# Kernel tuning notes

Measured on AMD Instinct MI355X. Metric: run time of the kernel, lower is better.

## Reference

```python
import jax, jax.numpy as jnp
import numpy as np

B, C, P, H, W = 8, 256, 64, 64, 64


def conv2d(x, w, b, pad):
    y = jax.lax.conv_general_dilated(
        x, w, window_strides=(1, 1), padding=[(pad, pad), (pad, pad)],
        dimension_numbers=("NCHW", "OIHW", "NCHW"))
    return y + b[None, :, None, None]


def setup_inputs() -> dict:
    key = jax.random.key(0)
    ks = jax.random.split(key, 9)
    x = jax.random.normal(ks[0], (B, C, H, W), dtype=jnp.float32)
    # conv weights, OIHW layout; scale ~ kaiming-ish
    w_top = jax.random.normal(ks[1], (P, C, 1, 1), jnp.float32) * (1.0 / np.sqrt(C))
    b_top = jnp.zeros((P,), jnp.float32)
    w_center = jax.random.normal(ks[2], (P, C, 1, 1), jnp.float32) * (1.0 / np.sqrt(C))
    b_center = jnp.zeros((P,), jnp.float32)
    w_bottom = jax.random.normal(ks[3], (C, C, 3, 3), jnp.float32) * (1.0 / np.sqrt(9 * C))
    b_bottom = jnp.zeros((C,), jnp.float32)
    w_out = jax.random.normal(ks[4], (C, C, 3, 3), jnp.float32) * (1.0 / np.sqrt(9 * C))
    b_out = jnp.zeros((C,), jnp.float32)
    return {"x": x, "w_top": w_top, "b_top": b_top, "w_center": w_center,
            "b_center": b_center, "w_bottom": w_bottom, "b_bottom": b_bottom,
            "w_out": w_out, "b_out": b_out}


def reference(x, w_top, b_top, w_center, b_center, w_bottom, b_bottom, w_out, b_out):
    b, c, h, w = x.shape
    hw = h * w
    x_top = conv2d(x, w_top, b_top, 0).reshape(b, -1, hw)          # [B, P, HW]
    x_center = conv2d(x, w_center, b_center, 0).reshape(b, -1, hw)  # [B, P, HW]
    x_center = jnp.swapaxes(x_center, 1, 2)                          # [B, HW, P]
    x_bottom = conv2d(x, w_bottom, b_bottom, 1).reshape(b, c, hw)
    x_bottom = jnp.swapaxes(x_bottom, 1, 2)                          # [B, HW, C]
    sp_map = jnp.einsum("bnp,bpm->bnm", x_center, x_top)            # [B, HW, HW]
    # NOTE: softmax is GLOBAL over the flattened HW*HW map per batch element,
    # not per-row (faithful to original Softmax(dim=1) on view(bsize, -1)).
    sp_map = jax.nn.softmax(sp_map.reshape(b, -1), axis=1).reshape(b, hw, hw)
    sp_map = jnp.einsum("bnm,bmc->bnc", sp_map, x_bottom)           # [B, HW, C]
    # NOTE: original does .reshape(b, C, h, w) on a [B, HW, C] tensor (no
    # transpose) -- replicate that exact memory reinterpretation.
    sp_map = sp_map.reshape(b, c, h, w)
    return conv2d(x + sp_map, w_out, b_out, 1)
```

## Files before the change

kernel.cpp:

```cpp
#include <hip/hip_runtime.h>
#include <hip/hip_bf16.h>
#include <type_traits>

constexpr int B_ = 8, C_ = 256, P_ = 64, H_ = 64, W_ = 64, HW_ = 4096;

typedef __attribute__((ext_vector_type(8))) short short8;
typedef __attribute__((ext_vector_type(4))) short short4v;
typedef __attribute__((ext_vector_type(4))) float f32x4;

__device__ __forceinline__ short bfbits(float f) {
    __hip_bfloat16 h = __float2bfloat16(f);
    return *reinterpret_cast<short*>(&h);
}
__device__ __forceinline__ float bf2f(short s) {
    __hip_bfloat16 h = *reinterpret_cast<__hip_bfloat16*>(&s);
    return (float)h;
}

#define GLL16(gsrc, ldst)                                                      \
    __builtin_amdgcn_global_load_lds(                                         \
        (const __attribute__((address_space(1))) void*)(gsrc),                \
        (__attribute__((address_space(3))) void*)(ldst), 16, 0, 0)


__global__ __launch_bounds__(256) void k_prep_w(
    const float* __restrict__ w, short8* __restrict__ wbP)
{
    const int idx = blockIdx.x * 256 + threadIdx.x;
    const int lane = idx & 63, cot = (idx >> 6) & 15;
    const int cb = (idx >> 10) & 7, tap = idx >> 13;
    const int lm = lane & 15, lq = lane >> 4;
    const int co = cot * 16 + lm, ci0 = cb * 32 + lq * 8;
    short8 v;
#pragma unroll
    for (int k = 0; k < 8; ++k)
        v[k] = bfbits(w[(co * 256 + ci0 + k) * 9 + tap]);
    wbP[idx] = v;
}

__global__ __launch_bounds__(256) void k_cvt_bf16(
    const float* __restrict__ x, short8* __restrict__ xB)
{
    const size_t i = ((size_t)blockIdx.x * 256 + threadIdx.x) * 16;
    short8 o[2];
#pragma unroll
    for (int q = 0; q < 2; ++q) {
#pragma unroll
        for (int j = 0; j < 2; ++j) {
            const float4 v = *reinterpret_cast<const float4*>(&x[i + q * 8 + j * 4]);
            o[q][j * 4 + 0] = bfbits(v.x);
            o[q][j * 4 + 1] = bfbits(v.y);
            o[q][j * 4 + 2] = bfbits(v.z);
            o[q][j * 4 + 3] = bfbits(v.w);
        }
    }
    short8* dp = (short8*)&xB[i >> 3];
    dp[0] = o[0];
    dp[1] = o[1];
}

__global__ __launch_bounds__(256) void k_pack_xb(
    const __hip_bfloat16* __restrict__ xb, short8* __restrict__ xbP)
{
    const int tid = blockIdx.x * 256 + threadIdx.x;
    const int lane = tid & 63, wid = tid >> 6;
    const int ct = wid & 15, g = (wid >> 4) & 127, b = wid >> 11;
    const int c = ct * 16 + (lane >> 2);
    const int mo = g * 32 + (lane & 3) * 8;
    const short8 v = *reinterpret_cast<const short8*>(
        &xb[((size_t)(b * 256 + c)) * HW_ + mo]);
    xbP[(size_t)wid * 64 + (lane & 3) * 16 + (lane >> 2)] = v;
}

__global__ __launch_bounds__(256) void k_conv1x1(
    const float* __restrict__ x,
    const float* __restrict__ w_top, const float* __restrict__ b_top,
    const float* __restrict__ w_cen, const float* __restrict__ b_cen,
    short8* __restrict__ xtPh, short8* __restrict__ xtPl,
    short8* __restrict__ xcPh, short8* __restrict__ xcPl)
{
    const int b = blockIdx.z;
    const int n = blockIdx.x * 256 + threadIdx.x;
    const int conv = blockIdx.y >> 2, pq = blockIdx.y & 3;
    const int p0 = pq * 16;
    const float* w    = conv ? w_cen : w_top;
    const float* bias = conv ? b_cen : b_top;
    short8* oh = conv ? xcPh : xtPh;
    short8* ol = conv ? xcPl : xtPl;

    const float* xp = x + (size_t)b * C_ * HW_ + n;
    float acc[16];
#pragma unroll
    for (int p = 0; p < 16; ++p) acc[p] = 0.f;

    for (int c = 0; c < C_; c += 4) {
        const float xv0 = xp[(size_t)(c + 0) * HW_];
        const float xv1 = xp[(size_t)(c + 1) * HW_];
        const float xv2 = xp[(size_t)(c + 2) * HW_];
        const float xv3 = xp[(size_t)(c + 3) * HW_];
#pragma unroll
        for (int p = 0; p < 16; ++p) {
            const float4 wv = *reinterpret_cast<const float4*>(&w[(p0 + p) * C_ + c]);
            float a = acc[p];
            a = fmaf(wv.x, xv0, a);
            a = fmaf(wv.y, xv1, a);
            a = fmaf(wv.z, xv2, a);
            a = fmaf(wv.w, xv3, a);
            acc[p] = a;
        }
    }
    const int nt = n >> 4, lmn = n & 15;
    const size_t obase = ((size_t)(b * 256 + nt) * 2 + (pq >> 1)) * 64 + lmn;
#pragma unroll
    for (int jj = 0; jj < 2; ++jj) {
        short8 vh, vl;
#pragma unroll
        for (int k = 0; k < 8; ++k) {
            const float v = acc[jj * 8 + k] + bias[p0 + jj * 8 + k];
            const short hb = bfbits(v);
            vh[k] = hb;
            vl[k] = bfbits(v - bf2f(hb));
        }
        const size_t idx = obase + (size_t)(((pq & 1) * 2 + jj) * 16);
        oh[idx] = vh;
        ol[idx] = vl;
    }
}

template <typename OT>
__global__ __launch_bounds__(512, 4) void k_conv3x3_mfma(
    const short* __restrict__ xin, const short8* __restrict__ wbP,
    const float* __restrict__ bias, OT* __restrict__ out)
{
    __shared__ __align__(16) short Xs[3][66][40];
    const int lin = blockIdx.x;
    const int b = lin & 7, h = lin >> 3;
    const int t = threadIdx.x;
    const int wave = t >> 6, lane = t & 63;
    const int lm = lane & 15, lq = lane >> 4;
    const int cobase = wave * 32;
    const int cot0 = wave * 2;

    f32x4 acc[4][2];
#pragma unroll
    for (int i = 0; i < 4; ++i)
#pragma unroll
        for (int j = 0; j < 2; ++j) acc[i][j] = f32x4{0.f, 0.f, 0.f, 0.f};

    if (t < 192) {
        const int r = t >> 6, cc = t & 31, side = (t >> 5) & 1;
        Xs[r][side ? 65 : 0][cc] = 0;
    }

    const short* xbase = xin + (size_t)b * C_ * HW_;

    for (int cb = 0; cb < 8; ++cb) {
        const int ci0 = cb * 32;
        __syncthreads();
#pragma unroll
        for (int it = 0; it < 3; ++it) {
            const int idx = it * 512 + t;
            const int r = idx >> 9, ci = (idx >> 4) & 31, wq = idx & 15;
            const int hh = h + r - 1;
            short4v v = {0, 0, 0, 0};
            if (hh >= 0 && hh < H_)
                v = *reinterpret_cast<const short4v*>(
                    &xbase[(size_t)(ci0 + ci) * HW_ + hh * W_ + wq * 4]);
            Xs[r][1 + wq * 4 + 0][ci] = v[0];
            Xs[r][1 + wq * 4 + 1][ci] = v[1];
            Xs[r][1 + wq * 4 + 2][ci] = v[2];
            Xs[r][1 + wq * 4 + 3][ci] = v[3];
        }
        __syncthreads();

#pragma unroll 3
        for (int tap = 0; tap < 9; ++tap) {
            const int dh = tap / 3;
            const int dw = tap % 3;
            const short8* wp = wbP + ((size_t)(tap * 8 + cb)) * 1024 + lane;
            short8 af[2];
            af[0] = wp[(cot0 + 0) * 64];
            af[1] = wp[(cot0 + 1) * 64];
            short8 bf[4];
#pragma unroll
            for (int nt = 0; nt < 4; ++nt)
                bf[nt] = *reinterpret_cast<const short8*>(
                    &Xs[dh][nt * 16 + lm + dw][lq * 8]);
#pragma unroll
            for (int nt = 0; nt < 4; ++nt)
#pragma unroll
                for (int ct = 0; ct < 2; ++ct)
                    acc[nt][ct] = __builtin_amdgcn_mfma_f32_16x16x32_bf16(
                        af[ct], bf[nt], acc[nt][ct], 0, 0, 0);
        }
    }

#pragma unroll
    for (int nt = 0; nt < 4; ++nt) {
        const int pos = h * W_ + nt * 16 + lm;
#pragma unroll
        for (int ct = 0; ct < 2; ++ct) {
            const int co = cobase + ct * 16 + lq * 4;
#pragma unroll
            for (int r = 0; r < 4; ++r) {
                const float v = acc[nt][ct][r] + bias[co + r];
                if constexpr (std::is_same<OT, __hip_bfloat16>::value)
                    out[((size_t)(b * C_ + co + r)) * HW_ + pos] = __float2bfloat16(v);
                else
                    out[((size_t)(b * C_ + co + r)) * HW_ + pos] = v;
            }
        }
    }
}

__global__ __launch_bounds__(512, 2) void k_attn_mfma(
    const short8* __restrict__ xtPh, const short8* __restrict__ xtPl,
    const short8* __restrict__ xcPh, const short8* __restrict__ xcPl,
    const short8* __restrict__ xbP, float* __restrict__ O,
    float* __restrict__ Z)
{
    extern __shared__ __align__(16) char smem[];
    short8* XTs = (short8*)smem;
    short8* XBs = (short8*)(smem + 32768);
    short8* Ps8 = (short8*)(smem + 98304);
    short4v* Ps4 = (short4v*)(smem + 98304);
    float* zred = (float*)(smem + 114688);

    const int lin = blockIdx.x;
    const int b = lin & 7, nblk = lin >> 3;
    const int n0 = nblk * 128;

    const int t = threadIdx.x, wv = t >> 6, lane = t & 63;
    const int lm = lane & 15, lq = lane >> 4;
    const int mh = wv >> 2, nq2 = wv & 3;
    const int nq = wv >> 2, cq = wv & 3;

    short8 cB2[2][2][2];
#pragma unroll
    for (int ntile = 0; ntile < 2; ++ntile) {
        const int gt = nblk * 8 + nq2 * 2 + ntile;
        const size_t base = ((size_t)(b * 256 + gt) * 2) * 64 + lane;
        cB2[ntile][0][0] = xcPh[base];
        cB2[ntile][1][0] = xcPh[base + 64];
        cB2[ntile][0][1] = xcPl[base];
        cB2[ntile][1][1] = xcPl[base + 64];
    }
    asm volatile("s_waitcnt vmcnt(0)" ::: "memory");

    auto stage = [&](int smt, int bufi) {
        short8* XT = XTs + bufi * 1024;
        short8* XB = XBs + bufi * 2048;
        const size_t abase = ((size_t)(b * 512 + smt * 8)) * 64;
#pragma unroll
        for (int k = 0; k < 2; ++k) {
            const int c = wv * 2 + k, ms = c >> 2, part = c & 3;
            const short8* src = (part < 2 ? xtPh : xtPl)
                                + abase + ms * 128 + (part & 1) * 64 + lane;
            GLL16(src, XT + c * 64);
        }
        const size_t p8 = ((size_t)(b * 2048 + smt * 32)) * 64;
#pragma unroll
        for (int k = 0; k < 4; ++k) {
            const int e = k * 512 + wv * 64;
            GLL16(xbP + p8 + e + lane, XB + e);
        }
    };
    stage(0, 0);

    f32x4 acc[4][4];
#pragma unroll
    for (int i = 0; i < 4; ++i)
#pragma unroll
        for (int jj = 0; jj < 4; ++jj) acc[i][jj] = f32x4{0.f, 0.f, 0.f, 0.f};
    float zp = 0.f;

    for (int mt = 0; mt < 64; ++mt) {
        const int cur = mt & 1;
        asm volatile("s_waitcnt vmcnt(4)" ::: "memory");
        __builtin_amdgcn_sched_barrier(0);
        __builtin_amdgcn_s_barrier();
        __builtin_amdgcn_sched_barrier(0);
        stage((mt + 1) & 63, cur ^ 1);

        const short8* XT = XTs + cur * 1024;
#pragma unroll
        for (int ms2 = 0; ms2 < 2; ++ms2) {
            const int ms = mh * 2 + ms2;
            const short8 aH0 = XT[(ms * 4 + 0) * 64 + lane];
            const short8 aH1 = XT[(ms * 4 + 1) * 64 + lane];
            const short8 aL0 = XT[(ms * 4 + 2) * 64 + lane];
            const short8 aL1 = XT[(ms * 4 + 3) * 64 + lane];
#pragma unroll
            for (int ntile = 0; ntile < 2; ++ntile) {
                f32x4 s = {0.f, 0.f, 0.f, 0.f};
                __builtin_amdgcn_s_setprio(1);
                s = __builtin_amdgcn_mfma_f32_16x16x32_bf16(aH0, cB2[ntile][0][0], s, 0, 0, 0);
                s = __builtin_amdgcn_mfma_f32_16x16x32_bf16(aH1, cB2[ntile][1][0], s, 0, 0, 0);
                s = __builtin_amdgcn_mfma_f32_16x16x32_bf16(aH0, cB2[ntile][0][1], s, 0, 0, 0);
                s = __builtin_amdgcn_mfma_f32_16x16x32_bf16(aH1, cB2[ntile][1][1], s, 0, 0, 0);
                s = __builtin_amdgcn_mfma_f32_16x16x32_bf16(aL0, cB2[ntile][0][0], s, 0, 0, 0);
                s = __builtin_amdgcn_mfma_f32_16x16x32_bf16(aL1, cB2[ntile][1][0], s, 0, 0, 0);
                __builtin_amdgcn_s_setprio(0);
                const float e0 = __expf(s[0]), e1 = __expf(s[1]);
                const float e2 = __expf(s[2]), e3 = __expf(s[3]);
                zp += (e0 + e1) + (e2 + e3);
                short4v pk = { bfbits(e0), bfbits(e1), bfbits(e2), bfbits(e3) };
                const int T = nq2 * 2 + ntile;
                const int lqp = (ms & 1) * 2 + (lq >> 1);
                Ps4[(((T * 2 + mh) * 64) + lqp * 16 + lm) * 2 + (lq & 1)] = pk;
            }
        }
        asm volatile("s_waitcnt vmcnt(6) lgkmcnt(0)" ::: "memory");
        __builtin_amdgcn_sched_barrier(0);
        __builtin_amdgcn_s_barrier();
        __builtin_amdgcn_sched_barrier(0);

        const short8* XB = XBs + cur * 2048;
        short8 vb0[4], vb1[4];
#pragma unroll
        for (int q4 = 0; q4 < 4; ++q4) {
            const int ct = cq * 4 + q4;
            vb0[q4] = XB[ct * 64 + lane];
            vb1[q4] = XB[1024 + ct * 64 + lane];
        }
#pragma unroll
        for (int nt2 = 0; nt2 < 4; ++nt2) {
            const int T = nq * 4 + nt2;
            const short8 pa0 = Ps8[(T * 2 + 0) * 64 + lane];
            const short8 pa1 = Ps8[(T * 2 + 1) * 64 + lane];
            __builtin_amdgcn_s_setprio(1);
#pragma unroll
            for (int q4 = 0; q4 < 4; ++q4) {
                acc[nt2][q4] = __builtin_amdgcn_mfma_f32_16x16x32_bf16(
                    pa0, vb0[q4], acc[nt2][q4], 0, 0, 0);
                acc[nt2][q4] = __builtin_amdgcn_mfma_f32_16x16x32_bf16(
                    pa1, vb1[q4], acc[nt2][q4], 0, 0, 0);
            }
            __builtin_amdgcn_s_setprio(0);
        }
    }

#pragma unroll
    for (int o = 32; o > 0; o >>= 1) zp += __shfl_down(zp, o, 64);
    if (lane == 0) zred[wv] = zp;
    __syncthreads();
    if (t == 0) {
        float zs = 0.f;
#pragma unroll
        for (int wvi = 0; wvi < 8; ++wvi) zs += zred[wvi];
        atomicAdd(&Z[b], zs);
    }

#pragma unroll
    for (int nt2 = 0; nt2 < 4; ++nt2) {
#pragma unroll
        for (int q4 = 0; q4 < 4; ++q4) {
            const int c = cq * 64 + q4 * 16 + lm;
#pragma unroll
            for (int r = 0; r < 4; ++r) {
                const int n = n0 + (nq * 4 + nt2) * 16 + lq * 4 + r;
                O[((size_t)b * HW_ + n) * C_ + c] = acc[nt2][q4][r];
            }
        }
    }
}

__global__ __launch_bounds__(256) void k_add_bf16(
    const float* __restrict__ x, const float* __restrict__ o,
    const float* __restrict__ Z, short4v* __restrict__ yB)
{
    const int bidx = blockIdx.x;
    const float invZ = 1.0f / Z[bidx >> 10];
    const size_t i = ((size_t)bidx * 256 + threadIdx.x) * 4;
    const float4 a = *reinterpret_cast<const float4*>(&x[i]);
    const float4 b = *reinterpret_cast<const float4*>(&o[i]);
    short4v r{bfbits(fmaf(b.x, invZ, a.x)), bfbits(fmaf(b.y, invZ, a.y)),
              bfbits(fmaf(b.z, invZ, a.z)), bfbits(fmaf(b.w, invZ, a.w))};
    yB[i >> 2] = r;
}

extern "C" void kernel_launch(void* const* d_in, const int* in_sizes, int n_in,
                              void* d_out, int out_size, void* d_ws, size_t ws_size,
                              hipStream_t stream)
{
    const float* x   = (const float*)d_in[0];
    const float* wt  = (const float*)d_in[1];
    const float* bt  = (const float*)d_in[2];
    const float* wc  = (const float*)d_in[3];
    const float* bc  = (const float*)d_in[4];
    const float* wbo = (const float*)d_in[5];
    const float* bbo = (const float*)d_in[6];
    const float* wo  = (const float*)d_in[7];
    const float* bo  = (const float*)d_in[8];
    float* out = (float*)d_out;

    uint8_t* w8 = (uint8_t*)d_ws;
    const size_t MB = 1u << 20;
    short8* xtPh = (short8*)(w8);
    short8* xtPl = (short8*)(w8 + 4 * MB);
    short8* xcPh = (short8*)(w8 + 8 * MB);
    short8* xcPl = (short8*)(w8 + 12 * MB);
    __hip_bfloat16* xbB = (__hip_bfloat16*)(w8 + 16 * MB);
    short8* xbP  = (short8*)(w8 + 32 * MB);
    float*  O    = (float*)(w8 + 48 * MB);
    short8* Wb1  = (short8*)(w8 + 48 * MB);
    short8* xB   = (short8*)(w8 + 64 * MB);
    short8* Wb2  = (short8*)(w8 + 32 * MB);
    short4v* yB  = (short4v*)(w8 + 16 * MB);
    float*  Z    = (float*)(w8 + 80 * MB);

    hipMemsetAsync(Z, 0, B_ * sizeof(float), stream);
    k_prep_w<<<dim3(288), 256, 0, stream>>>(wbo, Wb1);
    k_cvt_bf16<<<dim3(2048), 256, 0, stream>>>(x, xB);
    k_conv1x1<<<dim3(16, 8, 8), 256, 0, stream>>>(x, wt, bt, wc, bc,
                                                  xtPh, xtPl, xcPh, xcPl);
    k_conv3x3_mfma<__hip_bfloat16><<<dim3(512), 512, 0, stream>>>(
        (const short*)xB, Wb1, bbo, xbB);
    k_pack_xb<<<dim3(4096), 256, 0, stream>>>(xbB, xbP);
    k_attn_mfma<<<dim3(256), dim3(512), 114720, stream>>>(xtPh, xtPl, xcPh, xcPl,
                                                          xbP, O, Z);
    k_prep_w<<<dim3(288), 256, 0, stream>>>(wo, Wb2);
    k_add_bf16<<<dim3(8192), 256, 0, stream>>>(x, O, Z, yB);
    k_conv3x3_mfma<float><<<dim3(512), 512, 0, stream>>>(
        (const short*)yB, Wb2, bo, out);
}
```

Measured before the change: 390.0 us.

## Double-buffer conv3x3 LDS input tiles and fuse both 1x1 convs per thread

The 3x3 MFMA conv now keeps two LDS input buffers. It prefetches the next channel block into registers while MFMAs run on the current block, and syncs once per block instead of twice. This aims to hide global load latency behind compute, at the cost of doubled LDS and more registers. Separately, the 1x1 conv kernel computes the top and center projections in one thread so each x value is loaded once, which halves the grid and doubles the accumulators.

```diff
diff --git a/kernel.cpp b/kernel.cpp
--- a/kernel.cpp
+++ b/kernel.cpp
@@ -81,17 +81,13 @@
 {
     const int b = blockIdx.z;
     const int n = blockIdx.x * 256 + threadIdx.x;
-    const int conv = blockIdx.y >> 2, pq = blockIdx.y & 3;
+    const int pq = blockIdx.y;
     const int p0 = pq * 16;
-    const float* w    = conv ? w_cen : w_top;
-    const float* bias = conv ? b_cen : b_top;
-    short8* oh = conv ? xcPh : xtPh;
-    short8* ol = conv ? xcPl : xtPl;
 
     const float* xp = x + (size_t)b * C_ * HW_ + n;
-    float acc[16];
-#pragma unroll
-    for (int p = 0; p < 16; ++p) acc[p] = 0.f;
+    float acc0[16], acc1[16];
+#pragma unroll
+    for (int p = 0; p < 16; ++p) { acc0[p] = 0.f; acc1[p] = 0.f; }
 
     for (int c = 0; c < C_; c += 4) {
         const float xv0 = xp[(size_t)(c + 0) * HW_];
@@ -100,30 +96,37 @@
         const float xv3 = xp[(size_t)(c + 3) * HW_];
 #pragma unroll
         for (int p = 0; p < 16; ++p) {
-            const float4 wv = *reinterpret_cast<const float4*>(&w[(p0 + p) * C_ + c]);
-            float a = acc[p];
-            a = fmaf(wv.x, xv0, a);
-            a = fmaf(wv.y, xv1, a);
-            a = fmaf(wv.z, xv2, a);
-            a = fmaf(wv.w, xv3, a);
-            acc[p] = a;
+            const float4 wv0 = *reinterpret_cast<const float4*>(&w_top[(p0 + p) * C_ + c]);
+            const float4 wv1 = *reinterpret_cast<const float4*>(&w_cen[(p0 + p) * C_ + c]);
+            float a0 = acc0[p], a1 = acc1[p];
+            a0 = fmaf(wv0.x, xv0, a0);  a1 = fmaf(wv1.x, xv0, a1);
+            a0 = fmaf(wv0.y, xv1, a0);  a1 = fmaf(wv1.y, xv1, a1);
+            a0 = fmaf(wv0.z, xv2, a0);  a1 = fmaf(wv1.z, xv2, a1);
+            a0 = fmaf(wv0.w, xv3, a0);  a1 = fmaf(wv1.w, xv3, a1);
+            acc0[p] = a0;  acc1[p] = a1;
         }
     }
     const int nt = n >> 4, lmn = n & 15;
     const size_t obase = ((size_t)(b * 256 + nt) * 2 + (pq >> 1)) * 64 + lmn;
 #pragma unroll
     for (int jj = 0; jj < 2; ++jj) {
-        short8 vh, vl;
+        short8 vh0, vl0, vh1, vl1;
 #pragma unroll
         for (int k = 0; k < 8; ++k) {
-            const float v = acc[jj * 8 + k] + bias[p0 + jj * 8 + k];
-            const short hb = bfbits(v);
-            vh[k] = hb;
-            vl[k] = bfbits(v - bf2f(hb));
+            const float v0 = acc0[jj * 8 + k] + b_top[p0 + jj * 8 + k];
+            const short hb0 = bfbits(v0);
+            vh0[k] = hb0;
+            vl0[k] = bfbits(v0 - bf2f(hb0));
+            const float v1 = acc1[jj * 8 + k] + b_cen[p0 + jj * 8 + k];
+            const short hb1 = bfbits(v1);
+            vh1[k] = hb1;
+            vl1[k] = bfbits(v1 - bf2f(hb1));
         }
         const size_t idx = obase + (size_t)(((pq & 1) * 2 + jj) * 16);
-        oh[idx] = vh;
-        ol[idx] = vl;
+        xtPh[idx] = vh0;
+        xtPl[idx] = vl0;
+        xcPh[idx] = vh1;
+        xcPl[idx] = vl1;
     }
 }
 
@@ -132,7 +135,7 @@
     const short* __restrict__ xin, const short8* __restrict__ wbP,
     const float* __restrict__ bias, OT* __restrict__ out)
 {
-    __shared__ __align__(16) short Xs[3][66][40];
+    __shared__ __align__(16) short Xs[2][3][66][40];
     const int lin = blockIdx.x;
     const int b = lin & 7, h = lin >> 3;
     const int t = threadIdx.x;
@@ -147,16 +150,17 @@
 #pragma unroll
         for (int j = 0; j < 2; ++j) acc[i][j] = f32x4{0.f, 0.f, 0.f, 0.f};
 
-    if (t < 192) {
-        const int r = t >> 6, cc = t & 31, side = (t >> 5) & 1;
-        Xs[r][side ? 65 : 0][cc] = 0;
+    if (t < 384) {
+        const int bufi = t / 192, rem = t % 192;
+        const int r = rem >> 6, cc = rem & 31, side = (rem >> 5) & 1;
+        Xs[bufi][r][side ? 65 : 0][cc] = 0;
     }
 
     const short* xbase = xin + (size_t)b * C_ * HW_;
 
-    for (int cb = 0; cb < 8; ++cb) {
+    short4v pv[3];
+    auto gload = [&](int cb) {
         const int ci0 = cb * 32;
-        __syncthreads();
 #pragma unroll
         for (int it = 0; it < 3; ++it) {
             const int idx = it * 512 + t;
@@ -166,12 +170,28 @@
             if (hh >= 0 && hh < H_)
                 v = *reinterpret_cast<const short4v*>(
                     &xbase[(size_t)(ci0 + ci) * HW_ + hh * W_ + wq * 4]);
-            Xs[r][1 + wq * 4 + 0][ci] = v[0];
-            Xs[r][1 + wq * 4 + 1][ci] = v[1];
-            Xs[r][1 + wq * 4 + 2][ci] = v[2];
-            Xs[r][1 + wq * 4 + 3][ci] = v[3];
-        }
-        __syncthreads();
+            pv[it] = v;
+        }
+    };
+    auto lwrite = [&](int bufi) {
+#pragma unroll
+        for (int it = 0; it < 3; ++it) {
+            const int idx = it * 512 + t;
+            const int r = idx >> 9, ci = (idx >> 4) & 31, wq = idx & 15;
+            Xs[bufi][r][1 + wq * 4 + 0][ci] = pv[it][0];
+            Xs[bufi][r][1 + wq * 4 + 1][ci] = pv[it][1];
+            Xs[bufi][r][1 + wq * 4 + 2][ci] = pv[it][2];
+            Xs[bufi][r][1 + wq * 4 + 3][ci] = pv[it][3];
+        }
+    };
+
+    gload(0);
+    lwrite(0);
+    __syncthreads();
+
+    for (int cb = 0; cb < 8; ++cb) {
+        const int cur = cb & 1;
+        if (cb < 7) gload(cb + 1);
 
 #pragma unroll 3
         for (int tap = 0; tap < 9; ++tap) {
@@ -185,7 +205,7 @@
 #pragma unroll
             for (int nt = 0; nt < 4; ++nt)
                 bf[nt] = *reinterpret_cast<const short8*>(
-                    &Xs[dh][nt * 16 + lm + dw][lq * 8]);
+                    &Xs[cur][dh][nt * 16 + lm + dw][lq * 8]);
 #pragma unroll
             for (int nt = 0; nt < 4; ++nt)
 #pragma unroll
@@ -193,6 +213,9 @@
                     acc[nt][ct] = __builtin_amdgcn_mfma_f32_16x16x32_bf16(
                         af[ct], bf[nt], acc[nt][ct], 0, 0, 0);
         }
+
+        if (cb < 7) lwrite(cur ^ 1);
+        __syncthreads();
     }
 
 #pragma unroll
@@ -412,7 +435,7 @@
     hipMemsetAsync(Z, 0, B_ * sizeof(float), stream);
     k_prep_w<<<dim3(288), 256, 0, stream>>>(wbo, Wb1);
     k_cvt_bf16<<<dim3(2048), 256, 0, stream>>>(x, xB);
-    k_conv1x1<<<dim3(16, 8, 8), 256, 0, stream>>>(x, wt, bt, wc, bc,
+    k_conv1x1<<<dim3(16, 4, 8), 256, 0, stream>>>(x, wt, bt, wc, bc,
                                                   xtPh, xtPl, xcPh, xcPl);
     k_conv3x3_mfma<__hip_bfloat16><<<dim3(512), 512, 0, stream>>>(
         (const short*)xB, Wb1, bbo, xbB);
```

Measured after the change: 417.3 us. 7.0% more time.
